# Kernel optimization log

Measured on AMD Instinct MI355X. Metric: run time of the kernel, lower is better.

Reference implementation:

```python
import jax, jax.numpy as jnp
import numpy as np

Q_H, KV_H, DIM = 32, 8, 4096
HEAD_DIM = DIM // Q_H
FACTOR = Q_H // KV_H
BS, SL = 2, 2048


def setup_inputs() -> dict:
    key = jax.random.key(0)
    ks = jax.random.split(key, 9)
    s_in = 1.0 / np.sqrt(DIM)
    x = jax.random.normal(ks[0], (BS, SL, DIM), dtype=jnp.float32)
    wq_w = jax.random.uniform(ks[1], (DIM, Q_H * HEAD_DIM), jnp.float32, -s_in, s_in)
    wq_b = jax.random.uniform(ks[2], (Q_H * HEAD_DIM,), jnp.float32, -s_in, s_in)
    wk_w = jax.random.uniform(ks[3], (DIM, KV_H * HEAD_DIM), jnp.float32, -s_in, s_in)
    wk_b = jax.random.uniform(ks[4], (KV_H * HEAD_DIM,), jnp.float32, -s_in, s_in)
    wv_w = jax.random.uniform(ks[5], (DIM, KV_H * HEAD_DIM), jnp.float32, -s_in, s_in)
    wv_b = jax.random.uniform(ks[6], (KV_H * HEAD_DIM,), jnp.float32, -s_in, s_in)
    wo_w = jax.random.uniform(ks[7], (DIM, DIM), jnp.float32, -s_in, s_in)
    wo_b = jax.random.uniform(ks[8], (DIM,), jnp.float32, -s_in, s_in)
    return {"x": x, "wq_w": wq_w, "wq_b": wq_b, "wk_w": wk_w, "wk_b": wk_b,
            "wv_w": wv_w, "wv_b": wv_b, "wo_w": wo_w, "wo_b": wo_b}


def reference(x, wq_w, wq_b, wk_w, wk_b, wv_w, wv_b, wo_w, wo_b):
    bs, sl, _ = x.shape
    # projections
    q = (x @ wq_w + wq_b).reshape(bs, sl, Q_H, HEAD_DIM)          # [b,s,Hq,d]
    k = (x @ wk_w + wk_b).reshape(bs, sl, KV_H, HEAD_DIM)         # [b,s,Hkv,d]
    v = (x @ wv_w + wv_b).reshape(bs, sl, KV_H, HEAD_DIM)
    # group queries by kv head: [b,s,Hkv,factor,d]
    qg = q.reshape(bs, sl, KV_H, FACTOR, HEAD_DIM)
    scale = 1.0 / jnp.sqrt(jnp.asarray(HEAD_DIM, x.dtype))
    # scores: broadcast kv heads instead of physically repeating
    attn = jnp.einsum('bqhfd,bkhd->bhfqk', qg, k) * scale          # [b,Hkv,f,Sq,Sk]
    att = jax.nn.softmax(attn, axis=-1)
    a = jnp.einsum('bhfqk,bkhd->bqhfd', att, v)                    # [b,Sq,Hkv,f,d]
    a = a.reshape(bs, sl, DIM)
    return a @ wo_w + wo_b
```

## Files before the change

### kernel.cpp

```cpp
#include <hip/hip_runtime.h>
#include <math.h>


typedef unsigned short u16;
typedef unsigned int u32;
typedef __bf16 bf16x8 __attribute__((ext_vector_type(8)));
typedef float f32x4 __attribute__((ext_vector_type(4)));
typedef float f32x16 __attribute__((ext_vector_type(16)));
typedef unsigned short u16x8 __attribute__((ext_vector_type(8)));
typedef unsigned short u16x4 __attribute__((ext_vector_type(4)));
typedef int i32x2 __attribute__((ext_vector_type(2)));

#define MFMA16(a, b, c) __builtin_amdgcn_mfma_f32_16x16x32_bf16((a), (b), (c), 0, 0, 0)
#define MFMA32(a, b, c) __builtin_amdgcn_mfma_f32_32x32x16_bf16((a), (b), (c), 0, 0, 0)

#define GLDS(gp, lp)                                                      \
  __builtin_amdgcn_global_load_lds(                                       \
      (const __attribute__((address_space(1))) unsigned int*)(gp),        \
      (__attribute__((address_space(3))) unsigned int*)(lp), 16, 0, 0)

__device__ __forceinline__ u16 f2b(float f) {
  unsigned b = __float_as_uint(f);
  b += 0x7fffu + ((b >> 16) & 1u);
  return (u16)(b >> 16);
}

__device__ __forceinline__ u32 pk2(float a, float b) {
  union { __bf16 h[2]; u32 w; } u;
  u.h[0] = (__bf16)a;
  u.h[1] = (__bf16)b;
  return u.w;
}

__global__ __launch_bounds__(256) void cast_f32_bf16(const float* __restrict__ in,
                                                     u16* __restrict__ out, int n) {
  int i = (blockIdx.x * 256 + threadIdx.x) * 8;
  if (i >= n) return;
  f32x4 a = *(const f32x4*)&in[i];
  f32x4 b = *(const f32x4*)&in[i + 4];
  u16x8 v;
#pragma unroll
  for (int j = 0; j < 4; j++) { v[j] = f2b(a[j]); v[4 + j] = f2b(b[j]); }
  *(u16x8*)&out[i] = v;
}

__global__ __launch_bounds__(256) void transpose_cast(const float* __restrict__ in,
                                                      u16* __restrict__ out,
                                                      int R, int C) {
  __shared__ u16 t[32][33];
  const int lc = threadIdx.x & 31;
  const int lr = threadIdx.x >> 5;
  const int c0 = blockIdx.x * 32, r0 = blockIdx.y * 32;
#pragma unroll
  for (int i = 0; i < 4; i++) {
    int r = lr + i * 8;
    t[r][lc] = f2b(in[(size_t)(r0 + r) * C + c0 + lc]);
  }
  __syncthreads();
#pragma unroll
  for (int i = 0; i < 4; i++) {
    int r = lr + i * 8;
    out[(size_t)(c0 + r) * R + r0 + lc] = t[lc][r];
  }
}

template <int STORE_T, int OUT_F32>
__global__ __launch_bounds__(256, 2) void gemm_bt(const u16* __restrict__ A,
                                                  const u16* __restrict__ BT,
                                                  const float* __restrict__ bias,
                                                  void* __restrict__ Cv,
                                                  int M, int N) {
  __shared__ u16 As[128][64];
  __shared__ u16 Bs[128][64];
  const int tid = threadIdx.x;
  const int lane = tid & 63, wave = tid >> 6;
  const int l15 = lane & 15, quad = lane >> 4;
  const int m0 = blockIdx.y * 128, n0 = blockIdx.x * 128;
  const int wm = (wave >> 1) * 64, wn = (wave & 1) * 64;
  const int srow = wave * 32 + (lane >> 3);
  const int scol = (lane & 7) * 8;
  const u16* gA = &A[(size_t)(m0 + srow) * 4096 + scol];
  const u16* gB = &BT[(size_t)(n0 + srow) * 4096 + scol];
  f32x4 acc[4][4] = {};
  for (int kb = 0; kb < 4096; kb += 64) {
    __syncthreads();
#pragma unroll
    for (int j = 0; j < 4; j++) {
      GLDS(gA + (size_t)j * 8 * 4096 + kb, &As[wave * 32 + j * 8][0]);
      GLDS(gB + (size_t)j * 8 * 4096 + kb, &Bs[wave * 32 + j * 8][0]);
    }
    __syncthreads();
#pragma unroll
    for (int ks = 0; ks < 2; ks++) {
      bf16x8 a[4], b[4];
#pragma unroll
      for (int mt = 0; mt < 4; mt++)
        a[mt] = *(const bf16x8*)&As[wm + mt * 16 + l15][ks * 32 + quad * 8];
#pragma unroll
      for (int nt = 0; nt < 4; nt++)
        b[nt] = *(const bf16x8*)&Bs[wn + nt * 16 + l15][ks * 32 + quad * 8];
#pragma unroll
      for (int mt = 0; mt < 4; mt++)
#pragma unroll
        for (int nt = 0; nt < 4; nt++)
          acc[mt][nt] = MFMA16(a[mt], b[nt], acc[mt][nt]);
    }
  }
  float bv[4];
#pragma unroll
  for (int nt = 0; nt < 4; nt++) bv[nt] = bias[n0 + wn + nt * 16 + l15];
#pragma unroll
  for (int mt = 0; mt < 4; mt++) {
    const int row = m0 + wm + mt * 16 + quad * 4;
#pragma unroll
    for (int nt = 0; nt < 4; nt++) {
      const int col = n0 + wn + nt * 16 + l15;
      if (STORE_T) {
        u16x4 v;
#pragma unroll
        for (int r = 0; r < 4; r++) v[r] = f2b(acc[mt][nt][r] + bv[nt]);
        *(u16x4*)&((u16*)Cv)[(size_t)col * M + row] = v;
      } else if (OUT_F32) {
#pragma unroll
        for (int r = 0; r < 4; r++)
          ((float*)Cv)[(size_t)(row + r) * N + col] = acc[mt][nt][r] + bv[nt];
      } else {
#pragma unroll
        for (int r = 0; r < 4; r++)
          ((u16*)Cv)[(size_t)(row + r) * N + col] = f2b(acc[mt][nt][r] + bv[nt]);
      }
    }
  }
}

#define STAGE_K(kb, tt)                                                        \
  {                                                                            \
    _Pragma("unroll") for (int i_ = 0; i_ < 4; i_++)                           \
      GLDS(gK + (size_t)((tt) * 64 + i_ * 4) * 1024 + (offK ^ ((i_ & 1) << 5)),\
           &KsF[(kb) * 8192 + (wave * 16 + i_ * 4) * 128]);                    \
  }
#define STAGE_V(vb, tt)                                                        \
  {                                                                            \
    _Pragma("unroll") for (int i_ = 0; i_ < 4; i_++)                           \
      GLDS(gV + (size_t)(i_ * 8) * 4096 + (tt) * 64,                           \
           &VsF[(vb) * 8192 + (wave * 32 + i_ * 8) * 64]);                     \
  }

#define PV_STEP(pb)                                                            \
  {                                                                            \
    __builtin_amdgcn_s_setprio(1);                                             \
    _Pragma("unroll") for (int kvs = 0; kvs < 4; kvs++) {                      \
      union { u32 w[4]; bf16x8 v; } pa;                                        \
      pa.w[0] = fw[kvs][0]; pa.w[1] = fw[kvs][1];                              \
      pa.w[2] = fw[kvs][2]; pa.w[3] = fw[kvs][3];                              \
      _Pragma("unroll") for (int dt = 0; dt < 4; dt++) {                       \
        bf16x8 vf = *(const bf16x8*)&VsF[(pb) * 8192 + vOff[dt][kvs]];         \
        o[dt] = MFMA32(pa.v, vf, o[dt]);                                       \
      }                                                                        \
    }                                                                          \
    __builtin_amdgcn_s_setprio(0);                                             \
  }

__global__ __launch_bounds__(256, 2) void flash_gqa(const u16* __restrict__ K,
                                                    const u16* __restrict__ VT,
                                                    u16* __restrict__ QO) {
  __shared__ __align__(16) u16 KsF[2 * 64 * 128];
  __shared__ __align__(16) u16 VsF[3 * 128 * 64];
  const int tid = threadIdx.x;
  const int lane = tid & 63, wave = tid >> 6;
  const int l31 = lane & 31, hi = lane >> 5;
  const int bx = (blockIdx.x & 7) * 128 + (blockIdx.x >> 3);
  const int qt = bx & 15, h = (bx >> 4) & 31, b = bx >> 9;
  const int hk = h >> 2;
  const int qrow0 = b * 2048 + qt * 128 + wave * 32;
  const float scl2 = 0.08838834764831845f * 1.4426950408889634f;

  const int offK = ((lane & 15) * 8) ^ ((lane >> 4) << 3);
  const u16* gK = &K[(size_t)(b * 2048 + wave * 16 + (lane >> 4)) * 1024 + hk * 128];
  const u16* gV = &VT[(size_t)(hk * 128 + wave * 32 + (lane >> 3)) * 4096 + b * 2048 +
                      (((lane & 7) * 8) ^ ((lane >> 3) << 3))];

  int kOff[2][8], vOff[4][4];
#pragma unroll
  for (int kvt = 0; kvt < 2; kvt++) {
    const int row = kvt * 32 + l31;
#pragma unroll
    for (int ks = 0; ks < 8; ks++)
      kOff[kvt][ks] = row * 128 + ((ks * 16 + hi * 8) ^ ((row & 7) << 3));
  }
#pragma unroll
  for (int dt = 0; dt < 4; dt++) {
    const int row = dt * 32 + l31;
#pragma unroll
    for (int kvs = 0; kvs < 4; kvs++)
      vOff[dt][kvs] = row * 64 + ((kvs * 16 + hi * 8) ^ ((row & 7) << 3));
  }

  STAGE_K(0, 0);
  STAGE_V(0, 0);

  bf16x8 qf[8];
#pragma unroll
  for (int ks = 0; ks < 8; ks++)
    qf[ks] = *(const bf16x8*)&QO[(size_t)(qrow0 + l31) * 4096 + h * 128 + ks * 16 + hi * 8];

  f32x16 o[4] = {};
  float mrun = -3.0e38f, lrun = 0.0f;
  u32 fw[4][4];

  __syncthreads();

  for (int t = 0; t < 32; t++) {
    const int kb = t & 1;
    if (t < 31) {
      STAGE_K(kb ^ 1, t + 1);
      STAGE_V((t + 1) % 3, t + 1);
    }

    f32x16 st[2] = {};
    __builtin_amdgcn_s_setprio(1);
#pragma unroll
    for (int ks = 0; ks < 8; ks++) {
#pragma unroll
      for (int kvt = 0; kvt < 2; kvt++) {
        bf16x8 kf = *(const bf16x8*)&KsF[kb * 8192 + kOff[kvt][ks]];
        st[kvt] = MFMA32(kf, qf[ks], st[kvt]);
      }
    }
    __builtin_amdgcn_s_setprio(0);

    if (t > 0) PV_STEP((t - 1) % 3);

    float m8[8];
#pragma unroll
    for (int r = 0; r < 8; r++)
      m8[r] = fmaxf(fmaxf(fmaxf(st[0][r], st[0][r + 8]), st[1][r]), st[1][r + 8]);
    float mA = fmaxf(fmaxf(m8[0], m8[1]), m8[2]);
    mA = fmaxf(fmaxf(mA, m8[3]), m8[4]);
    mA = fmaxf(fmaxf(mA, m8[5]), m8[6]);
    mA = fmaxf(mA, m8[7]);
    i32x2 mr = __builtin_amdgcn_permlane32_swap(__float_as_int(mA), __float_as_int(mA),
                                                false, false);
    const float mx = fmaxf(__int_as_float(mr[0]), __int_as_float(mr[1]));
    const float mxs = mx * scl2;
    if (__any(mxs > mrun + 8.0f)) {
      const float mn = fmaxf(mrun, mxs);
      const float alpha = __builtin_amdgcn_exp2f(mrun - mn);
      mrun = mn;
      lrun *= alpha;
#pragma unroll
      for (int re = 0; re < 16; re++) {
        const float av = __shfl(alpha, (re & 3) + 8 * (re >> 2) + 4 * hi, 64);
#pragma unroll
        for (int dt = 0; dt < 4; dt++) o[dt][re] *= av;
      }
    }
    float rsa[4] = {0.f, 0.f, 0.f, 0.f};
#pragma unroll
    for (int kvt = 0; kvt < 2; kvt++)
#pragma unroll
      for (int r = 0; r < 16; r++) {
        const float p = __builtin_amdgcn_exp2f(fmaf(st[kvt][r], scl2, -mrun));
        st[kvt][r] = p;
        rsa[r & 3] += p;
      }
    float rs = (rsa[0] + rsa[1]) + (rsa[2] + rsa[3]);
    i32x2 rr = __builtin_amdgcn_permlane32_swap(__float_as_int(rs), __float_as_int(rs),
                                                false, false);
    lrun += __int_as_float(rr[0]) + __int_as_float(rr[1]);

    u32 W0[8], W1[8];
#pragma unroll
    for (int rp = 0; rp < 8; rp++) {
      W0[rp] = pk2(st[0][2 * rp], st[0][2 * rp + 1]);
      W1[rp] = pk2(st[1][2 * rp], st[1][2 * rp + 1]);
    }
#pragma unroll
    for (int kvs = 0; kvs < 4; kvs++) {
#pragma unroll
      for (int sl = 0; sl < 2; sl++) {
        const u32 wa = (kvs < 2) ? W0[4 * (kvs & 1) + sl] : W1[4 * (kvs & 1) + sl];
        const u32 wb = (kvs < 2) ? W0[4 * (kvs & 1) + 2 + sl] : W1[4 * (kvs & 1) + 2 + sl];
        i32x2 r = __builtin_amdgcn_permlane32_swap((int)wa, (int)wb, false, false);
        fw[kvs][sl] = (u32)r[0];
        fw[kvs][2 + sl] = (u32)r[1];
      }
    }

    __syncthreads();
  }

  PV_STEP(1);

  const float invl = 1.0f / lrun;
#pragma unroll
  for (int re = 0; re < 16; re++) {
    const int qv = (re & 3) + 8 * (re >> 2) + 4 * hi;
    const float il = __shfl(invl, qv, 64);
    const size_t rowb = (size_t)(qrow0 + qv) * 4096 + h * 128;
#pragma unroll
    for (int dt = 0; dt < 4; dt++)
      QO[rowb + dt * 32 + l31] = f2b(o[dt][re] * il);
  }
}

extern "C" void kernel_launch(void* const* d_in, const int* in_sizes, int n_in,
                              void* d_out, int out_size, void* d_ws, size_t ws_size,
                              hipStream_t stream) {
  (void)in_sizes; (void)n_in; (void)out_size; (void)ws_size;
  const float* x    = (const float*)d_in[0];
  const float* wq_w = (const float*)d_in[1];
  const float* wq_b = (const float*)d_in[2];
  const float* wk_w = (const float*)d_in[3];
  const float* wk_b = (const float*)d_in[4];
  const float* wv_w = (const float*)d_in[5];
  const float* wv_b = (const float*)d_in[6];
  const float* wo_w = (const float*)d_in[7];
  const float* wo_b = (const float*)d_in[8];
  float* out = (float*)d_out;
  char* ws = (char*)d_ws;
  char* od = (char*)d_out;

  u16* TQ  = (u16*)(ws);
  u16* QA  = (u16*)(ws + 33554432);
  u16* Xb  = (u16*)(od);
  u16* TK  = (u16*)(od + 33554432);
  u16* TV  = (u16*)(od + 41943040);
  u16* Kb  = (u16*)(od + 50331648);
  u16* VTb = (u16*)(od + 58720256);

  cast_f32_bf16<<<8192, 256, 0, stream>>>(x, Xb, 16777216);
  transpose_cast<<<dim3(128, 128), 256, 0, stream>>>(wq_w, TQ, 4096, 4096);
  transpose_cast<<<dim3(32, 128), 256, 0, stream>>>(wk_w, TK, 4096, 1024);
  transpose_cast<<<dim3(32, 128), 256, 0, stream>>>(wv_w, TV, 4096, 1024);

  gemm_bt<0, 0><<<dim3(32, 32), 256, 0, stream>>>(Xb, TQ, wq_b, QA, 4096, 4096);
  gemm_bt<0, 0><<<dim3(8, 32), 256, 0, stream>>>(Xb, TK, wk_b, Kb, 4096, 1024);
  gemm_bt<1, 0><<<dim3(8, 32), 256, 0, stream>>>(Xb, TV, wv_b, VTb, 4096, 1024);

  transpose_cast<<<dim3(128, 128), 256, 0, stream>>>(wo_w, TQ, 4096, 4096);

  flash_gqa<<<dim3(1024), 256, 0, stream>>>(Kb, VTb, QA);

  gemm_bt<0, 1><<<dim3(32, 32), 256, 0, stream>>>(QA, TQ, wo_b, out, 4096, 4096);
}
```

Baseline: 857.4 us.

## Add 256x256-tile 8-wave GEMM with staged LDS pipeline for Q and output projections

Adds a new GEMM kernel that computes 256x256 output tiles with 512 threads and a double-buffered LDS. Global-to-LDS loads are interleaved between four MFMA quadrants with barriers and priority hints, and the block index is swizzled across XCDs. It replaces the 128-tile gemm_bt for the two 4096x4096x4096 projections. The aim is more data reuse per tile and better overlap of loads with MFMA work, at the cost of a larger LDS footprint and a more fragile hand-counted vmcnt schedule.

```diff
diff --git a/kernel.cpp b/kernel.cpp
--- a/kernel.cpp
+++ b/kernel.cpp
@@ -133,6 +133,149 @@
   }
 }
 
+#define STA256(bb, s, tt)                                                     \
+  {                                                                           \
+    _Pragma("unroll") for (int j_ = 0; j_ < 2; j_++) {                        \
+      const int r_ = (w >> 2) * 128 + (s) * 64 + (w & 3) * 16 + j_ * 8;       \
+      GLDS(gAu + (size_t)r_ * 4096 + (size_t)(tt) * 64,                       \
+           &Lds[((bb) * 2 + 0) * 16384 + r_ * 64]);                           \
+    }                                                                         \
+  }
+#define STB256(bb, s, tt)                                                     \
+  {                                                                           \
+    _Pragma("unroll") for (int j_ = 0; j_ < 2; j_++) {                        \
+      const int r_ = (w >> 1) * 64 + (s) * 32 + (w & 1) * 16 + j_ * 8;        \
+      GLDS(gBu + (size_t)r_ * 4096 + (size_t)(tt) * 64,                       \
+           &Lds[((bb) * 2 + 1) * 16384 + r_ * 64]);                           \
+    }                                                                         \
+  }
+
+#define QUAD256(MB, NB)                                                       \
+  {                                                                           \
+    _Pragma("unroll") for (int mt_ = 0; mt_ < 4; mt_++)                       \
+        _Pragma("unroll") for (int nt_ = 0; nt_ < 2; nt_++) {                 \
+      acc[(MB) * 4 + mt_][(NB) * 2 + nt_] = MFMA16(                           \
+          a[mt_][0], b[(NB) * 2 + nt_][0], acc[(MB) * 4 + mt_][(NB) * 2 + nt_]); \
+      acc[(MB) * 4 + mt_][(NB) * 2 + nt_] = MFMA16(                           \
+          a[mt_][1], b[(NB) * 2 + nt_][1], acc[(MB) * 4 + mt_][(NB) * 2 + nt_]); \
+    }                                                                         \
+  }
+
+template <int OUT_F32>
+__global__ __launch_bounds__(512, 2) void gemm256(const u16* __restrict__ A,
+                                                  const u16* __restrict__ BT,
+                                                  const float* __restrict__ bias,
+                                                  void* __restrict__ Cv) {
+  __shared__ __align__(16) u16 Lds[2 * 2 * 16384];
+  const int tid = threadIdx.x;
+  const int lane = tid & 63, w = tid >> 6;
+  const int l15 = lane & 15, quad = lane >> 4;
+  const int wr = w >> 2, wc = w & 3;
+  const int bid = (blockIdx.x & 7) * 32 + (blockIdx.x >> 3);
+  const int m0 = (bid >> 4) * 256, n0 = (bid & 15) * 256;
+
+  const int srow = lane >> 3;
+  const int schunk = ((lane & 7) ^ srow) * 8;
+  const u16* gAu = &A[(size_t)(m0 + srow) * 4096 + schunk];
+  const u16* gBu = &BT[(size_t)(n0 + srow) * 4096 + schunk];
+
+  const int sw0 = ((quad ^ (l15 & 7)) * 8), sw1 = (((4 + quad) ^ (l15 & 7)) * 8);
+  const int aoff0 = (wr * 128 + l15) * 64 + sw0, aoff1 = (wr * 128 + l15) * 64 + sw1;
+  const int boff0 = (wc * 64 + l15) * 64 + sw0, boff1 = (wc * 64 + l15) * 64 + sw1;
+
+  f32x4 acc[8][4] = {};
+  bf16x8 a[4][2], b[4][2];
+
+  STA256(0, 0, 0);
+  STB256(0, 0, 0);
+  STB256(0, 1, 0);
+  STA256(0, 1, 0);
+  STA256(1, 0, 1);
+  STB256(1, 0, 1);
+  STB256(1, 1, 1);
+  asm volatile("s_waitcnt vmcnt(6)" ::: "memory");
+  __builtin_amdgcn_s_barrier();
+
+  for (int u = 0; u < 64; u++) {
+    const int cur = u & 1;
+    const u16* LA = &Lds[(cur * 2 + 0) * 16384];
+    const u16* LB = &Lds[(cur * 2 + 1) * 16384];
+
+#pragma unroll
+    for (int mt = 0; mt < 4; mt++) {
+      a[mt][0] = *(const bf16x8*)&LA[aoff0 + mt * 1024];
+      a[mt][1] = *(const bf16x8*)&LA[aoff1 + mt * 1024];
+    }
+#pragma unroll
+    for (int nt = 0; nt < 2; nt++) {
+      b[nt][0] = *(const bf16x8*)&LB[boff0 + nt * 1024];
+      b[nt][1] = *(const bf16x8*)&LB[boff1 + nt * 1024];
+    }
+    if (u < 63) STA256(cur ^ 1, 1, u + 1);
+    __builtin_amdgcn_s_barrier();
+    asm volatile("s_waitcnt lgkmcnt(0)" ::: "memory");
+    __builtin_amdgcn_s_setprio(1);
+    QUAD256(0, 0);
+    __builtin_amdgcn_s_setprio(0);
+    __builtin_amdgcn_s_barrier();
+
+#pragma unroll
+    for (int nt = 2; nt < 4; nt++) {
+      b[nt][0] = *(const bf16x8*)&LB[boff0 + nt * 1024];
+      b[nt][1] = *(const bf16x8*)&LB[boff1 + nt * 1024];
+    }
+    if (u < 62) STA256(cur, 0, u + 2);
+    __builtin_amdgcn_s_barrier();
+    asm volatile("s_waitcnt lgkmcnt(0)" ::: "memory");
+    __builtin_amdgcn_s_setprio(1);
+    QUAD256(0, 1);
+    __builtin_amdgcn_s_setprio(0);
+    __builtin_amdgcn_s_barrier();
+
+#pragma unroll
+    for (int mt = 0; mt < 4; mt++) {
+      a[mt][0] = *(const bf16x8*)&LA[aoff0 + (mt + 4) * 1024];
+      a[mt][1] = *(const bf16x8*)&LA[aoff1 + (mt + 4) * 1024];
+    }
+    if (u < 62) STB256(cur, 0, u + 2);
+    __builtin_amdgcn_s_barrier();
+    asm volatile("s_waitcnt lgkmcnt(0)" ::: "memory");
+    __builtin_amdgcn_s_setprio(1);
+    QUAD256(1, 0);
+    __builtin_amdgcn_s_setprio(0);
+    __builtin_amdgcn_s_barrier();
+
+    if (u < 62) STB256(cur, 1, u + 2);
+    __builtin_amdgcn_s_setprio(1);
+    QUAD256(1, 1);
+    __builtin_amdgcn_s_setprio(0);
+    if (u == 62) asm volatile("s_waitcnt vmcnt(0)" ::: "memory");
+    else if (u < 62) asm volatile("s_waitcnt vmcnt(6)" ::: "memory");
+    if (u < 63) __builtin_amdgcn_s_barrier();
+  }
+
+  float bv[4];
+#pragma unroll
+  for (int nt = 0; nt < 4; nt++) bv[nt] = bias[n0 + wc * 64 + nt * 16 + l15];
+#pragma unroll
+  for (int mt = 0; mt < 8; mt++) {
+    const int row = m0 + wr * 128 + mt * 16 + quad * 4;
+#pragma unroll
+    for (int nt = 0; nt < 4; nt++) {
+      const int col = n0 + wc * 64 + nt * 16 + l15;
+      if (OUT_F32) {
+#pragma unroll
+        for (int r = 0; r < 4; r++)
+          ((float*)Cv)[(size_t)(row + r) * 4096 + col] = acc[mt][nt][r] + bv[nt];
+      } else {
+#pragma unroll
+        for (int r = 0; r < 4; r++)
+          ((u16*)Cv)[(size_t)(row + r) * 4096 + col] = f2b(acc[mt][nt][r] + bv[nt]);
+      }
+    }
+  }
+}
+
 #define STAGE_K(kb, tt)                                                        \
   {                                                                            \
     _Pragma("unroll") for (int i_ = 0; i_ < 4; i_++)                           \
@@ -334,7 +477,7 @@
   transpose_cast<<<dim3(32, 128), 256, 0, stream>>>(wk_w, TK, 4096, 1024);
   transpose_cast<<<dim3(32, 128), 256, 0, stream>>>(wv_w, TV, 4096, 1024);
 
-  gemm_bt<0, 0><<<dim3(32, 32), 256, 0, stream>>>(Xb, TQ, wq_b, QA, 4096, 4096);
+  gemm256<0><<<256, 512, 0, stream>>>(Xb, TQ, wq_b, QA);
   gemm_bt<0, 0><<<dim3(8, 32), 256, 0, stream>>>(Xb, TK, wk_b, Kb, 4096, 1024);
   gemm_bt<1, 0><<<dim3(8, 32), 256, 0, stream>>>(Xb, TV, wv_b, VTb, 4096, 1024);
 
@@ -342,5 +485,5 @@
 
   flash_gqa<<<dim3(1024), 256, 0, stream>>>(Kb, VTb, QA);
 
-  gemm_bt<0, 1><<<dim3(32, 32), 256, 0, stream>>>(QA, TQ, wo_b, out, 4096, 4096);
-}
+  gemm256<1><<<256, 512, 0, stream>>>(QA, TQ, wo_b, out);
+}
```

Result: faster. 777.4 us (-9.3%).
